# Kernel tuning notes

Measured on AMD Instinct MI355X. Metric: run time of the kernel, lower is better.

Reference implementation:

```python
import jax, jax.numpy as jnp
import numpy as np

N_NODES = 50000
N_EDGES = 800000
IN_DIM, HID_DIM, OUT_DIM = 512, 64, 40
DROPOUT_P = 0.5


def _gcn_conv(h, src, dst, deg_inv_sqrt, W, b, n_nodes):
    # PyG GCNConv (normalize=True, add_self_loops=True):
    #   h' = h @ W; out[dst] += d^-1/2[src] * d^-1/2[dst] * h'[src]; out += b
    # src/dst already include self-loops; deg_inv_sqrt precomputed from them.
    ht = h @ W                                            # [N, F_out]
    norm = deg_inv_sqrt[src] * deg_inv_sqrt[dst]          # [E+N]
    msg = ht[src] * norm[:, None]                         # [E+N, F_out]
    out = jax.ops.segment_sum(msg, dst, num_segments=n_nodes)
    return out + b


def setup_inputs() -> dict:
    key = jax.random.key(0)
    k1, k2, k3, k4 = jax.random.split(key, 4)
    x = jax.random.normal(k1, (N_NODES, IN_DIM), dtype=jnp.float32)
    edge_index = jax.random.randint(k2, (2, N_EDGES), 0, N_NODES, dtype=jnp.int32)
    W1 = jax.random.normal(k3, (IN_DIM, HID_DIM), dtype=jnp.float32) / np.sqrt(IN_DIM)
    b1 = jnp.zeros((HID_DIM,), dtype=jnp.float32)
    W2 = jax.random.normal(k4, (HID_DIM, OUT_DIM), dtype=jnp.float32) / np.sqrt(HID_DIM)
    b2 = jnp.zeros((OUT_DIM,), dtype=jnp.float32)
    return {"x": x, "edge_index": edge_index, "W1": W1, "b1": b1, "W2": W2, "b2": b2}


def reference(x, edge_index, W1, b1, W2, b2):
    n = x.shape[0]
    loop = jnp.arange(n, dtype=edge_index.dtype)
    src = jnp.concatenate([edge_index[0], loop])          # add self-loops
    dst = jnp.concatenate([edge_index[1], loop])
    deg = jax.ops.segment_sum(jnp.ones_like(dst, dtype=x.dtype), dst, num_segments=n)
    deg_inv_sqrt = jnp.where(deg > 0, jax.lax.rsqrt(deg), 0.0)

    h = _gcn_conv(x, src, dst, deg_inv_sqrt, W1, b1, n)
    h = jax.nn.relu(h)
    # dropout (training=True) with a fixed key for determinism
    keep = jax.random.bernoulli(jax.random.key(42), 1.0 - DROPOUT_P, h.shape)
    h = jnp.where(keep, h / (1.0 - DROPOUT_P), 0.0)
    h = _gcn_conv(h, src, dst, deg_inv_sqrt, W2, b2, n)
    return jax.nn.log_softmax(h, axis=1)
```

## Files before the change

kernel.cpp:

```cpp
#include <hip/hip_runtime.h>
#include <math.h>
#include <float.h>

#define N_NODES 50000
#define N_EDGES 800000
#define IN_DIM  512
#define HID_DIM 64
#define OUT_DIM 40
#define GEMM1_BLOCKS 782
#define FILL_BLOCKS 1568
#define NODES_PER_GRP 6250
#define BCAP 96

typedef __attribute__((ext_vector_type(8))) short bf16x8;
typedef __attribute__((ext_vector_type(4))) float f32x4;

__device__ __forceinline__ unsigned rotl32(unsigned v, int n) {
  return (v << n) | (v >> (32 - n));
}

__device__ __forceinline__ void threefry2x32_0_42(unsigned x0, unsigned x1,
                                                  unsigned &o0, unsigned &o1) {
  const unsigned ks0 = 0u;
  const unsigned ks1 = 42u;
  const unsigned ks2 = 0u ^ 42u ^ 0x1BD11BDAu;
  x0 += ks0; x1 += ks1;
  x0 += x1; x1 = rotl32(x1, 13); x1 ^= x0;
  x0 += x1; x1 = rotl32(x1, 15); x1 ^= x0;
  x0 += x1; x1 = rotl32(x1, 26); x1 ^= x0;
  x0 += x1; x1 = rotl32(x1,  6); x1 ^= x0;
  x0 += ks1; x1 += ks2 + 1u;
  x0 += x1; x1 = rotl32(x1, 17); x1 ^= x0;
  x0 += x1; x1 = rotl32(x1, 29); x1 ^= x0;
  x0 += x1; x1 = rotl32(x1, 16); x1 ^= x0;
  x0 += x1; x1 = rotl32(x1, 24); x1 ^= x0;
  x0 += ks2; x1 += ks0 + 2u;
  x0 += x1; x1 = rotl32(x1, 13); x1 ^= x0;
  x0 += x1; x1 = rotl32(x1, 15); x1 ^= x0;
  x0 += x1; x1 = rotl32(x1, 26); x1 ^= x0;
  x0 += x1; x1 = rotl32(x1,  6); x1 ^= x0;
  x0 += ks0; x1 += ks1 + 3u;
  x0 += x1; x1 = rotl32(x1, 17); x1 ^= x0;
  x0 += x1; x1 = rotl32(x1, 29); x1 ^= x0;
  x0 += x1; x1 = rotl32(x1, 16); x1 ^= x0;
  x0 += x1; x1 = rotl32(x1, 24); x1 ^= x0;
  x0 += ks1; x1 += ks2 + 4u;
  x0 += x1; x1 = rotl32(x1, 13); x1 ^= x0;
  x0 += x1; x1 = rotl32(x1, 15); x1 ^= x0;
  x0 += x1; x1 = rotl32(x1, 26); x1 ^= x0;
  x0 += x1; x1 = rotl32(x1,  6); x1 ^= x0;
  x0 += ks2; x1 += ks0 + 5u;
  o0 = x0; o1 = x1;
}

__device__ __forceinline__ unsigned short f2bf(float f) {
  unsigned u = __float_as_uint(f);
  unsigned r = u + 0x7FFFu + ((u >> 16) & 1u);
  return (unsigned short)(r >> 16);
}

__global__ void k_init(const float* __restrict__ W1, const float* __restrict__ W2,
                       unsigned short* __restrict__ Wb1, float* __restrict__ w2t,
                       int* __restrict__ cnt) {
  int i = blockIdx.x * 256 + threadIdx.x;
  if (i < N_NODES) cnt[i] = 0;
  if (i < IN_DIM * HID_DIM) {
    int j = i & 7;
    int lane = (i >> 3) & 63;
    int cg = (i >> 9) & 3;
    int kb = i >> 11;
    int k = kb * 32 + ((lane >> 4) << 3) + j;
    int c = cg * 16 + (lane & 15);
    Wb1[i] = f2bf(W1[k * HID_DIM + c]);
  }
  if (i < HID_DIM * OUT_DIM) {
    int j = i >> 6;
    int k = i & 63;
    w2t[i] = W2[k * OUT_DIM + j];
  }
}

#define XS 136
__global__ __launch_bounds__(512) void k_gemm1_fill(
    const int* __restrict__ ei, int* __restrict__ cnt,
    unsigned short* __restrict__ elist2,
    const float* __restrict__ x, const unsigned short* __restrict__ Wb1,
    unsigned short* __restrict__ ht1b) {
  __shared__ unsigned short sxa[2][64 * XS];

  if (blockIdx.x >= GEMM1_BLOCKS) {
    const int fb = blockIdx.x - GEMM1_BLOCKS;
    const int grp = blockIdx.x & 7;
    const int ord = fb >> 3;
    const int lo = grp * NODES_PER_GRP;
    const int hi = lo + NODES_PER_GRP;
    for (int e = ord * 512 + threadIdx.x; e < N_EDGES; e += 196 * 512) {
      int d = ei[N_EDGES + e];
      if (d >= lo && d < hi) {
        int s = ei[e];
        int slot = atomicAdd(&cnt[d], 1);
        if (slot < BCAP) elist2[d * BCAP + slot] = (unsigned short)s;
      }
    }
    return;
  }

  const int tid = threadIdx.x;
  const int lane = tid & 63;
  const int wave = tid >> 6;
  const int brow = blockIdx.x * 64;
  const int sr = tid >> 3;
  const int sq = tid & 7;

  f32x4 acc[2];
  acc[0] = (f32x4){0.f, 0.f, 0.f, 0.f};
  acc[1] = (f32x4){0.f, 0.f, 0.f, 0.f};

  const bf16x8* __restrict__ Wv = (const bf16x8*)Wb1;
  int gr = brow + sr;
  if (gr >= N_NODES) gr = N_NODES - 1;
  const float* __restrict__ xrow = x + (size_t)gr * IN_DIM;

  float4 lv[4];
#define LOADR(K0)                                                             \
  {                                                                           \
    _Pragma("unroll")                                                         \
    for (int j = 0; j < 4; ++j)                                               \
      lv[j] = *(const float4*)(xrow + (K0) + (sq + j * 8) * 4);               \
  }
#define WRITE(B)                                                              \
  {                                                                           \
    _Pragma("unroll")                                                         \
    for (int j = 0; j < 4; ++j) {                                             \
      ushort4 o;                                                              \
      o.x = f2bf(lv[j].x); o.y = f2bf(lv[j].y);                               \
      o.z = f2bf(lv[j].z); o.w = f2bf(lv[j].w);                               \
      *(ushort4*)(&sxa[B][sr * XS + (sq + j * 8) * 4]) = o;                   \
    }                                                                         \
  }

  LOADR(0)
  WRITE(0)
  __syncthreads();

  const int arow = (16 * (wave & 3) + (lane & 15)) * XS + ((lane >> 4) << 3);
  const int cgb = 2 * (wave >> 2);

  int buf = 0;
  for (int kc = 0; kc < 4; ++kc) {
    if (kc < 3) LOADR((kc + 1) * 128)
#pragma unroll
    for (int ks = 0; ks < 4; ++ks) {
      bf16x8 a = *(const bf16x8*)(&sxa[buf][arow + ks * 32]);
      int kb = kc * 4 + ks;
#pragma unroll
      for (int c = 0; c < 2; ++c) {
        bf16x8 b = Wv[(kb * 4 + cgb + c) * 64 + lane];
        acc[c] = __builtin_amdgcn_mfma_f32_16x16x32_bf16(a, b, acc[c], 0, 0, 0);
      }
    }
    if (kc < 3) WRITE(buf ^ 1)
    __syncthreads();
    buf ^= 1;
  }
#undef LOADR
#undef WRITE

#pragma unroll
  for (int q = 0; q < 4; ++q) {
    int grow = brow + 16 * (wave & 3) + ((lane >> 4) << 2) + q;
    if (grow < N_NODES) {
#pragma unroll
      for (int c = 0; c < 2; ++c) {
        ht1b[(size_t)grow * HID_DIM + (cgb + c) * 16 + (lane & 15)] =
            f2bf(acc[c][q]);
      }
    }
  }
}

__global__ __launch_bounds__(256) void k_agg1g2(const int* __restrict__ cnt,
                                                const unsigned short* __restrict__ elist2,
                                                const unsigned short* __restrict__ ht1b,
                                                const float* __restrict__ b1,
                                                const float* __restrict__ w2t,
                                                unsigned short* __restrict__ ht2b) {
  const int wave = threadIdx.x >> 6;
  const int lane = threadIdx.x & 63;
  const int d = blockIdx.x * 4 + wave;
  const int g = lane >> 3;
  const int fh = lane & 7;

  unsigned t0, t1;
  threefry2x32_0_42(0u, (unsigned)d * 64u + (unsigned)lane, t0, t1);
  unsigned long long keep = __ballot(!((t0 ^ t1) & 0x80000000u));

  int cn = cnt[d];
  if (cn > BCAP) cn = BCAP;
  const unsigned short* __restrict__ bucket = elist2 + d * BCAP;
  float4 a0 = {0.f, 0.f, 0.f, 0.f};
  float4 a1 = {0.f, 0.f, 0.f, 0.f};
#pragma unroll 2
  for (int j = g; j < cn; j += 8) {
    int s = bucket[j];
    float ds = rsqrtf((float)cnt[s] + 1.0f);
    const uint2* __restrict__ p = (const uint2*)(ht1b + (size_t)s * HID_DIM);
    uint2 q0 = p[fh];
    uint2 q1 = p[fh + 8];
    a0.x += __uint_as_float(q0.x << 16) * ds;
    a0.y += __uint_as_float(q0.x & 0xFFFF0000u) * ds;
    a0.z += __uint_as_float(q0.y << 16) * ds;
    a0.w += __uint_as_float(q0.y & 0xFFFF0000u) * ds;
    a1.x += __uint_as_float(q1.x << 16) * ds;
    a1.y += __uint_as_float(q1.x & 0xFFFF0000u) * ds;
    a1.z += __uint_as_float(q1.y << 16) * ds;
    a1.w += __uint_as_float(q1.y & 0xFFFF0000u) * ds;
  }
#pragma unroll
  for (int m = 32; m >= 8; m >>= 1) {
    a0.x += __shfl_xor(a0.x, m); a0.y += __shfl_xor(a0.y, m);
    a0.z += __shfl_xor(a0.z, m); a0.w += __shfl_xor(a0.w, m);
    a1.x += __shfl_xor(a1.x, m); a1.y += __shfl_xor(a1.y, m);
    a1.z += __shfl_xor(a1.z, m); a1.w += __shfl_xor(a1.w, m);
  }

  float dd = rsqrtf((float)cn + 1.0f);
  {
    const uint2* __restrict__ ps = (const uint2*)(ht1b + (size_t)d * HID_DIM);
    uint2 s0 = ps[fh];
    uint2 s1 = ps[fh + 8];
    a0.x += __uint_as_float(s0.x << 16) * dd;
    a0.y += __uint_as_float(s0.x & 0xFFFF0000u) * dd;
    a0.z += __uint_as_float(s0.y << 16) * dd;
    a0.w += __uint_as_float(s0.y & 0xFFFF0000u) * dd;
    a1.x += __uint_as_float(s1.x << 16) * dd;
    a1.y += __uint_as_float(s1.x & 0xFFFF0000u) * dd;
    a1.z += __uint_as_float(s1.y << 16) * dd;
    a1.w += __uint_as_float(s1.y & 0xFFFF0000u) * dd;
  }
  float4 bb0 = *(const float4*)(b1 + fh * 4);
  float4 bb1 = *(const float4*)(b1 + fh * 4 + 32);
  int f0 = fh * 4;
  float4 v0, v1;
  v0.x = fmaxf(a0.x * dd + bb0.x, 0.f) * (((keep >> (f0 + 0)) & 1) ? 2.f : 0.f);
  v0.y = fmaxf(a0.y * dd + bb0.y, 0.f) * (((keep >> (f0 + 1)) & 1) ? 2.f : 0.f);
  v0.z = fmaxf(a0.z * dd + bb0.z, 0.f) * (((keep >> (f0 + 2)) & 1) ? 2.f : 0.f);
  v0.w = fmaxf(a0.w * dd + bb0.w, 0.f) * (((keep >> (f0 + 3)) & 1) ? 2.f : 0.f);
  v1.x = fmaxf(a1.x * dd + bb1.x, 0.f) * (((keep >> (f0 + 32)) & 1) ? 2.f : 0.f);
  v1.y = fmaxf(a1.y * dd + bb1.y, 0.f) * (((keep >> (f0 + 33)) & 1) ? 2.f : 0.f);
  v1.z = fmaxf(a1.z * dd + bb1.z, 0.f) * (((keep >> (f0 + 34)) & 1) ? 2.f : 0.f);
  v1.w = fmaxf(a1.w * dd + bb1.w, 0.f) * (((keep >> (f0 + 35)) & 1) ? 2.f : 0.f);

  const int jb = g * 5;
  float part[5];
#pragma unroll
  for (int c = 0; c < 5; ++c) {
    const float* __restrict__ wr = w2t + (jb + c) * 64;
    float4 wA = *(const float4*)(wr + f0);
    float4 wB = *(const float4*)(wr + 32 + f0);
    part[c] = v0.x * wA.x + v0.y * wA.y + v0.z * wA.z + v0.w * wA.w +
              v1.x * wB.x + v1.y * wB.y + v1.z * wB.z + v1.w * wB.w;
  }
#pragma unroll
  for (int c = 0; c < 5; ++c) {
    part[c] += __shfl_xor(part[c], 1);
    part[c] += __shfl_xor(part[c], 2);
    part[c] += __shfl_xor(part[c], 4);
  }
  if (fh == 0) {
#pragma unroll
    for (int c = 0; c < 5; ++c)
      ht2b[(size_t)d * OUT_DIM + jb + c] = f2bf(part[c] * dd);
  }
}

__global__ __launch_bounds__(256) void k_agg2(const int* __restrict__ cnt,
                                              const unsigned short* __restrict__ elist2,
                                              const unsigned short* __restrict__ ht2b,
                                              const float* __restrict__ b2,
                                              float* __restrict__ out) {
  const int wave = threadIdx.x >> 6;
  const int lane = threadIdx.x & 63;
  const int d = blockIdx.x * 4 + wave;
  const int g = lane >> 3;
  const int fh = lane & 7;
  const bool extra = fh < 2;

  int cn = cnt[d];
  if (cn > BCAP) cn = BCAP;
  const unsigned short* __restrict__ bucket = elist2 + d * BCAP;
  float4 a0 = {0.f, 0.f, 0.f, 0.f};
  float4 a1 = {0.f, 0.f, 0.f, 0.f};
#pragma unroll 2
  for (int j = g; j < cn; j += 8) {
    int s = bucket[j];
    const uint2* __restrict__ p = (const uint2*)(ht2b + (size_t)s * OUT_DIM);
    uint2 q0 = p[fh];
    a0.x += __uint_as_float(q0.x << 16);
    a0.y += __uint_as_float(q0.x & 0xFFFF0000u);
    a0.z += __uint_as_float(q0.y << 16);
    a0.w += __uint_as_float(q0.y & 0xFFFF0000u);
    if (extra) {
      uint2 q1 = p[8 + fh];
      a1.x += __uint_as_float(q1.x << 16);
      a1.y += __uint_as_float(q1.x & 0xFFFF0000u);
      a1.z += __uint_as_float(q1.y << 16);
      a1.w += __uint_as_float(q1.y & 0xFFFF0000u);
    }
  }
#pragma unroll
  for (int m = 32; m >= 8; m >>= 1) {
    a0.x += __shfl_xor(a0.x, m); a0.y += __shfl_xor(a0.y, m);
    a0.z += __shfl_xor(a0.z, m); a0.w += __shfl_xor(a0.w, m);
    a1.x += __shfl_xor(a1.x, m); a1.y += __shfl_xor(a1.y, m);
    a1.z += __shfl_xor(a1.z, m); a1.w += __shfl_xor(a1.w, m);
  }

  {
    const uint2* __restrict__ ps = (const uint2*)(ht2b + (size_t)d * OUT_DIM);
    uint2 s0 = ps[fh];
    a0.x += __uint_as_float(s0.x << 16);
    a0.y += __uint_as_float(s0.x & 0xFFFF0000u);
    a0.z += __uint_as_float(s0.y << 16);
    a0.w += __uint_as_float(s0.y & 0xFFFF0000u);
    if (extra) {
      uint2 s1 = ps[8 + fh];
      a1.x += __uint_as_float(s1.x << 16);
      a1.y += __uint_as_float(s1.x & 0xFFFF0000u);
      a1.z += __uint_as_float(s1.y << 16);
      a1.w += __uint_as_float(s1.y & 0xFFFF0000u);
    }
  }

  float dd = rsqrtf((float)cn + 1.0f);
  float4 bb0 = *(const float4*)(b2 + fh * 4);
  float4 v0, v1;
  v0.x = a0.x * dd + bb0.x;
  v0.y = a0.y * dd + bb0.y;
  v0.z = a0.z * dd + bb0.z;
  v0.w = a0.w * dd + bb0.w;
  float mm = fmaxf(fmaxf(v0.x, v0.y), fmaxf(v0.z, v0.w));
  if (extra) {
    float4 bb1 = *(const float4*)(b2 + 32 + fh * 4);
    v1.x = a1.x * dd + bb1.x;
    v1.y = a1.y * dd + bb1.y;
    v1.z = a1.z * dd + bb1.z;
    v1.w = a1.w * dd + bb1.w;
    mm = fmaxf(mm, fmaxf(fmaxf(v1.x, v1.y), fmaxf(v1.z, v1.w)));
  }
  mm = fmaxf(mm, __shfl_xor(mm, 1));
  mm = fmaxf(mm, __shfl_xor(mm, 2));
  mm = fmaxf(mm, __shfl_xor(mm, 4));
  float e = expf(v0.x - mm) + expf(v0.y - mm) + expf(v0.z - mm) + expf(v0.w - mm);
  if (extra)
    e += expf(v1.x - mm) + expf(v1.y - mm) + expf(v1.z - mm) + expf(v1.w - mm);
  e += __shfl_xor(e, 1);
  e += __shfl_xor(e, 2);
  e += __shfl_xor(e, 4);
  float ls = logf(e) + mm;

  if (g == 0) {
    float4 r;
    r.x = v0.x - ls; r.y = v0.y - ls; r.z = v0.z - ls; r.w = v0.w - ls;
    *(float4*)(out + (size_t)d * OUT_DIM + fh * 4) = r;
    if (extra) {
      float4 r1;
      r1.x = v1.x - ls; r1.y = v1.y - ls; r1.z = v1.z - ls; r1.w = v1.w - ls;
      *(float4*)(out + (size_t)d * OUT_DIM + 32 + fh * 4) = r1;
    }
  }
}

extern "C" void kernel_launch(void* const* d_in, const int* in_sizes, int n_in,
                              void* d_out, int out_size, void* d_ws, size_t ws_size,
                              hipStream_t stream) {
  const float* x  = (const float*)d_in[0];
  const int*   ei = (const int*)  d_in[1];
  const float* W1 = (const float*)d_in[2];
  const float* b1 = (const float*)d_in[3];
  const float* W2 = (const float*)d_in[4];
  const float* b2 = (const float*)d_in[5];
  float* out = (float*)d_out;
  float* ws  = (float*)d_ws;

  unsigned short* ht1b = (unsigned short*)ws;
  unsigned short* ht2b = (unsigned short*)(ws + 1600000);
  unsigned short* Wb1 = (unsigned short*)(ws + 2600000);
  float* w2t  = ws + 2620000;
  int* cnt    = (int*)(ws + 2630000);
  unsigned short* elist2 = (unsigned short*)(ws + 2681200);

  k_init<<<196, 256, 0, stream>>>(W1, W2, Wb1, w2t, cnt);
  k_gemm1_fill<<<GEMM1_BLOCKS + FILL_BLOCKS, 512, 0, stream>>>(ei, cnt, elist2,
                                                               x, Wb1, ht1b);
  k_agg1g2<<<12500, 256, 0, stream>>>(cnt, elist2, ht1b, b1, w2t, ht2b);
  k_agg2<<<12500, 256, 0, stream>>>(cnt, elist2, ht2b, b2, out);
}
```

Baseline: 131.0 us.

## Remap aggregation blocks to XCD-local node groups and batch fill-edge loads

The fill loop now loads all eight of a thread's destination indices up front instead of one per iteration, so the global loads can overlap. The aggregation kernels remap block IDs so that block index mod 8 picks a contiguous node group of 6250. This matches how the fill phase partitioned nodes by group, so each XCD's L2 should already hold the cnt and bucket lines it wrote. The cost is a few idle waves in the padded last blocks and a block-to-XCD mapping assumption that depends on the hardware scheduler.

After: 131.9 us. No clear change (+0.7%).

```diff
diff --git a/kernel.cpp b/kernel.cpp
--- a/kernel.cpp
+++ b/kernel.cpp
@@ -11,6 +11,8 @@
 #define FILL_BLOCKS 1568
 #define NODES_PER_GRP 6250
 #define BCAP 96
+#define AGG_Q 1563
+#define AGG_BLOCKS (8 * AGG_Q)
 
 typedef __attribute__((ext_vector_type(8))) short bf16x8;
 typedef __attribute__((ext_vector_type(4))) float f32x4;
@@ -94,12 +96,19 @@
     const int ord = fb >> 3;
     const int lo = grp * NODES_PER_GRP;
     const int hi = lo + NODES_PER_GRP;
-    for (int e = ord * 512 + threadIdx.x; e < N_EDGES; e += 196 * 512) {
-      int d = ei[N_EDGES + e];
-      if (d >= lo && d < hi) {
-        int s = ei[e];
-        int slot = atomicAdd(&cnt[d], 1);
-        if (slot < BCAP) elist2[d * BCAP + slot] = (unsigned short)s;
+    const int ebase = ord * 512 + threadIdx.x;
+    int dv[8];
+#pragma unroll
+    for (int i = 0; i < 8; ++i) {
+      int e = ebase + i * (196 * 512);
+      dv[i] = (e < N_EDGES) ? ei[N_EDGES + e] : -1;
+    }
+#pragma unroll
+    for (int i = 0; i < 8; ++i) {
+      if (dv[i] >= lo && dv[i] < hi) {
+        int s = ei[ebase + i * (196 * 512)];
+        int slot = atomicAdd(&cnt[dv[i]], 1);
+        if (slot < BCAP) elist2[dv[i] * BCAP + slot] = (unsigned short)s;
       }
     }
     return;
@@ -187,7 +196,9 @@
                                                 unsigned short* __restrict__ ht2b) {
   const int wave = threadIdx.x >> 6;
   const int lane = threadIdx.x & 63;
-  const int d = blockIdx.x * 4 + wave;
+  const int dl = (blockIdx.x >> 3) * 4 + wave;
+  if (dl >= NODES_PER_GRP) return;
+  const int d = (blockIdx.x & 7) * NODES_PER_GRP + dl;
   const int g = lane >> 3;
   const int fh = lane & 7;
 
@@ -281,7 +292,9 @@
                                               float* __restrict__ out) {
   const int wave = threadIdx.x >> 6;
   const int lane = threadIdx.x & 63;
-  const int d = blockIdx.x * 4 + wave;
+  const int dl = (blockIdx.x >> 3) * 4 + wave;
+  if (dl >= NODES_PER_GRP) return;
+  const int d = (blockIdx.x & 7) * NODES_PER_GRP + dl;
   const int g = lane >> 3;
   const int fh = lane & 7;
   const bool extra = fh < 2;
@@ -393,6 +406,6 @@
   k_init<<<196, 256, 0, stream>>>(W1, W2, Wb1, w2t, cnt);
   k_gemm1_fill<<<GEMM1_BLOCKS + FILL_BLOCKS, 512, 0, stream>>>(ei, cnt, elist2,
                                                                x, Wb1, ht1b);
-  k_agg1g2<<<12500, 256, 0, stream>>>(cnt, elist2, ht1b, b1, w2t, ht2b);
-  k_agg2<<<12500, 256, 0, stream>>>(cnt, elist2, ht2b, b2, out);
-}
+  k_agg1g2<<<AGG_BLOCKS, 256, 0, stream>>>(cnt, elist2, ht1b, b1, w2t, ht2b);
+  k_agg2<<<AGG_BLOCKS, 256, 0, stream>>>(cnt, elist2, ht2b, b2, out);
+}
```
